# Kernel tuning notes

Hardware: AMD Instinct MI355X
Metric: run time of the kernel (lower is better)

Reference implementation:

```python
import jax, jax.numpy as jnp
import numpy as np

B, S, IN_F, OUT_F = 4, 2048, 4096, 4096
ALPHA = 0.01

def setup_inputs() -> dict:
    key = jax.random.key(0)
    k1, k2 = jax.random.split(key, 2)
    # int8-valued activations and weights (stored as int32 per harness dtype)
    x = jax.random.randint(k1, (B, S, IN_F), -127, 127, dtype=jnp.int32)
    weight = jax.random.randint(k2, (IN_F, OUT_F), -127, 127, dtype=jnp.int32)
    bias = jnp.zeros((1, OUT_F), dtype=jnp.float16)
    alpha = jnp.full((1,), ALPHA, dtype=jnp.float32)
    return {"x": x, "weight": weight, "bias": bias, "alpha": alpha}

def reference(x, weight, bias, alpha):
    # Faithful to forward's default (non-hybrid) path:
    # y = F.linear(x.float(), weight.t().float(), bias.float()) * alpha
    # F.linear(x, W^T) == x @ W, with W shape (in_features, out_features).
    x_shape = x.shape
    xf = x.reshape(-1, x_shape[-1]).astype(jnp.float32)          # [B*S, in]
    wf = weight.astype(jnp.float32)                               # [in, out]
    y = (xf @ wf + bias.astype(jnp.float32)) * alpha              # [B*S, out]
    return y.reshape(*x_shape[:-1], -1)                           # [B, S, out]
```

## Files before the change

kernel.cpp:

```cpp
#include <hip/hip_runtime.h>
#include <hip/hip_fp16.h>

using i32x4  = __attribute__((ext_vector_type(4)))  int;
using i32x16 = __attribute__((ext_vector_type(16))) int;

static constexpr int M  = 4 * 2048;
static constexpr int N  = 4096;
static constexpr int K  = 4096;
static constexpr int BM = 256, BN = 128, BK = 64;
static constexpr int NT = K / BK;
static constexpr int ATILE = BM * BK;
static constexpr int BTILE = BN * BK;


__device__ __forceinline__ unsigned pack4(i32x4 v) {
  return (unsigned)((v.x & 255) | ((v.y & 255) << 8) | ((v.z & 255) << 16) | (v.w << 24));
}

__global__ __launch_bounds__(256) void pack_x_kernel(const int* __restrict__ x,
                                                     unsigned char* __restrict__ wa) {
  unsigned g = blockIdx.x * 256 + threadIdx.x;
  unsigned row = g & 255;
  unsigned kg  = (g >> 8) & 3;
  unsigned kt  = (g >> 10) & 63;
  unsigned br  = g >> 16;
  const int* src = x + ((size_t)(br * 256 + row) * K + kt * 64 + kg * 16);
  i32x4 v0 = *(const i32x4*)(src + 0);
  i32x4 v1 = *(const i32x4*)(src + 4);
  i32x4 v2 = *(const i32x4*)(src + 8);
  i32x4 v3 = *(const i32x4*)(src + 12);
  i32x4 d;
  d.x = (int)pack4(v0); d.y = (int)pack4(v1); d.z = (int)pack4(v2); d.w = (int)pack4(v3);
  *(i32x4*)(wa + (size_t)g * 16) = d;
}

__global__ __launch_bounds__(256) void pack_w_kernel(const int* __restrict__ w,
                                                     unsigned char* __restrict__ wb) {
  unsigned g = blockIdx.x * 256 + threadIdx.x;
  unsigned col = g & 127;
  unsigned kg  = (g >> 7) & 3;
  unsigned kt  = (g >> 9) & 63;
  unsigned bn  = g >> 15;
  unsigned n   = bn * 128 + col;
  unsigned k0  = kt * 64 + kg * 16;
  const int* src = w + (size_t)k0 * N + n;
  i32x4 d;
#pragma unroll
  for (int j = 0; j < 4; ++j) {
    int b0 = src[(size_t)(j * 4 + 0) * N];
    int b1 = src[(size_t)(j * 4 + 1) * N];
    int b2 = src[(size_t)(j * 4 + 2) * N];
    int b3 = src[(size_t)(j * 4 + 3) * N];
    d[j] = (b0 & 255) | ((b1 & 255) << 8) | ((b2 & 255) << 16) | (b3 << 24);
  }
  *(i32x4*)(wb + (size_t)g * 16) = d;
}


__device__ __forceinline__ void gload_lds16(const void* g, void* l) {
  __builtin_amdgcn_global_load_lds((const __attribute__((address_space(1))) unsigned int*)g,
                                   (__attribute__((address_space(3))) unsigned int*)l,
                                   16, 0, 0);
}

__global__ __launch_bounds__(256, 2) void gemm_i8(const unsigned char* __restrict__ wa,
                                                  const unsigned char* __restrict__ wb,
                                                  const __half* __restrict__ bias,
                                                  const float* __restrict__ alphaP,
                                                  float* __restrict__ out) {
  __shared__ __align__(16) unsigned char As[3][ATILE];
  __shared__ __align__(16) unsigned char Bs[3][BTILE];

  const int tid  = threadIdx.x;
  const int lane = tid & 63;
  const int w    = tid >> 6;
  const int wr   = w >> 1, wc = w & 1;
  const int l31  = lane & 31;
  const int kgl  = lane >> 5;

  const int bc = blockIdx.x;
  const int br = blockIdx.y;

  const unsigned char* ga = wa + (size_t)br * NT * ATILE;
  const unsigned char* gb = wb + (size_t)bc * NT * BTILE;

  auto stage = [&](int buf, int t) {
    const unsigned char* at = ga + (size_t)t * ATILE;
    const unsigned char* bt = gb + (size_t)t * BTILE;
#pragma unroll
    for (int j = 0; j < 4; ++j)
      gload_lds16(at + (w * 4 + j) * 1024 + lane * 16, &As[buf][(w * 4 + j) * 1024]);
#pragma unroll
    for (int j = 0; j < 2; ++j)
      gload_lds16(bt + (w * 2 + j) * 1024 + lane * 16, &Bs[buf][(w * 2 + j) * 1024]);
  };

  stage(0, 0);
  stage(1, 1);
  asm volatile("s_waitcnt vmcnt(6)" ::: "memory");
  __builtin_amdgcn_s_barrier();

  i32x16 acc[4][2] = {};

  const int arow = wr * 128 + l31;
  const int bcol = wc * 64 + l31;

  for (int t = 0; t < NT; ++t) {
    if (t + 2 < NT) stage((t + 2) % 3, t + 2);

    const unsigned char* Ab = &As[t % 3][0] + kgl * 4096;
    const unsigned char* Bb = &Bs[t % 3][0] + kgl * 2048;

#pragma unroll
    for (int kc = 0; kc < 2; ++kc) {
      const unsigned char* Ap = Ab + kc * 8192;
      const unsigned char* Bp = Bb + kc * 4096;
      i32x4 a0 = *(const i32x4*)(Ap + (arow +  0) * 16);
      i32x4 a1 = *(const i32x4*)(Ap + (arow + 32) * 16);
      i32x4 a2 = *(const i32x4*)(Ap + (arow + 64) * 16);
      i32x4 a3 = *(const i32x4*)(Ap + (arow + 96) * 16);
      i32x4 b0 = *(const i32x4*)(Bp + (bcol +  0) * 16);
      i32x4 b1 = *(const i32x4*)(Bp + (bcol + 32) * 16);
      acc[0][0] = __builtin_amdgcn_mfma_i32_32x32x32_i8(a0, b0, acc[0][0], 0, 0, 0);
      acc[0][1] = __builtin_amdgcn_mfma_i32_32x32x32_i8(a0, b1, acc[0][1], 0, 0, 0);
      acc[1][0] = __builtin_amdgcn_mfma_i32_32x32x32_i8(a1, b0, acc[1][0], 0, 0, 0);
      acc[1][1] = __builtin_amdgcn_mfma_i32_32x32x32_i8(a1, b1, acc[1][1], 0, 0, 0);
      acc[2][0] = __builtin_amdgcn_mfma_i32_32x32x32_i8(a2, b0, acc[2][0], 0, 0, 0);
      acc[2][1] = __builtin_amdgcn_mfma_i32_32x32x32_i8(a2, b1, acc[2][1], 0, 0, 0);
      acc[3][0] = __builtin_amdgcn_mfma_i32_32x32x32_i8(a3, b0, acc[3][0], 0, 0, 0);
      acc[3][1] = __builtin_amdgcn_mfma_i32_32x32x32_i8(a3, b1, acc[3][1], 0, 0, 0);
    }

    if (t + 2 < NT)      asm volatile("s_waitcnt vmcnt(6)" ::: "memory");
    else if (t + 1 < NT) asm volatile("s_waitcnt vmcnt(0)" ::: "memory");
    __builtin_amdgcn_s_barrier();
  }

  const float alpha = *alphaP;
  const int row0 = br * 256 + wr * 128 + 4 * kgl;
  const int col0 = bc * 128 + wc * 64 + l31;
#pragma unroll
  for (int ni = 0; ni < 2; ++ni) {
    const int col = col0 + ni * 32;
    const float bf = __half2float(bias[col]);
#pragma unroll
    for (int mi = 0; mi < 4; ++mi) {
#pragma unroll
      for (int r = 0; r < 16; ++r) {
        const int row = row0 + mi * 32 + (r & 3) + 8 * (r >> 2);
        out[(size_t)row * N + col] = ((float)acc[mi][ni][r] + bf) * alpha;
      }
    }
  }
}

extern "C" void kernel_launch(void* const* d_in, const int* in_sizes, int n_in,
                              void* d_out, int out_size, void* d_ws, size_t ws_size,
                              hipStream_t stream) {
  const int*    x     = (const int*)d_in[0];
  const int*    wgt   = (const int*)d_in[1];
  const __half* bias  = (const __half*)d_in[2];
  const float*  alpha = (const float*)d_in[3];
  float*        out   = (float*)d_out;

  unsigned char* wa = (unsigned char*)d_ws;
  unsigned char* wb = wa + (size_t)M * K;

  pack_x_kernel<<<(M * (size_t)K / 16) / 256, 256, 0, stream>>>(x, wa);
  pack_w_kernel<<<(N * (size_t)K / 16) / 256, 256, 0, stream>>>(wgt, wb);

  dim3 grid(N / BN, M / BM);
  gemm_i8<<<grid, 256, 0, stream>>>(wa, wb, bias, alpha, out);
}
```

Measured before the change: 242.4 us.

## Replace direct-to-LDS triple buffering with register-staged double buffering; merge pack kernels

```diff
diff --git a/kernel.cpp b/kernel.cpp
--- a/kernel.cpp
+++ b/kernel.cpp
@@ -12,64 +12,61 @@
 static constexpr int ATILE = BM * BK;
 static constexpr int BTILE = BN * BK;
 
+static constexpr int PX_BLOCKS = (int)((size_t)M * K / 16 / 256);
+static constexpr int PW_BLOCKS = (int)((size_t)N * K / 16 / 256);
 
 __device__ __forceinline__ unsigned pack4(i32x4 v) {
   return (unsigned)((v.x & 255) | ((v.y & 255) << 8) | ((v.z & 255) << 16) | (v.w << 24));
 }
 
-__global__ __launch_bounds__(256) void pack_x_kernel(const int* __restrict__ x,
-                                                     unsigned char* __restrict__ wa) {
-  unsigned g = blockIdx.x * 256 + threadIdx.x;
-  unsigned row = g & 255;
-  unsigned kg  = (g >> 8) & 3;
-  unsigned kt  = (g >> 10) & 63;
-  unsigned br  = g >> 16;
-  const int* src = x + ((size_t)(br * 256 + row) * K + kt * 64 + kg * 16);
-  i32x4 v0 = *(const i32x4*)(src + 0);
-  i32x4 v1 = *(const i32x4*)(src + 4);
-  i32x4 v2 = *(const i32x4*)(src + 8);
-  i32x4 v3 = *(const i32x4*)(src + 12);
-  i32x4 d;
-  d.x = (int)pack4(v0); d.y = (int)pack4(v1); d.z = (int)pack4(v2); d.w = (int)pack4(v3);
-  *(i32x4*)(wa + (size_t)g * 16) = d;
+__global__ __launch_bounds__(256) void pack_kernel(const int* __restrict__ x,
+                                                   const int* __restrict__ w,
+                                                   unsigned char* __restrict__ wa,
+                                                   unsigned char* __restrict__ wb) {
+  if (blockIdx.x < PX_BLOCKS) {
+    unsigned g = blockIdx.x * 256 + threadIdx.x;
+    unsigned row = g & 255;
+    unsigned kg  = (g >> 8) & 3;
+    unsigned kt  = (g >> 10) & 63;
+    unsigned br  = g >> 16;
+    const int* src = x + ((size_t)(br * 256 + row) * K + kt * 64 + kg * 16);
+    i32x4 v0 = *(const i32x4*)(src + 0);
+    i32x4 v1 = *(const i32x4*)(src + 4);
+    i32x4 v2 = *(const i32x4*)(src + 8);
+    i32x4 v3 = *(const i32x4*)(src + 12);
+    i32x4 d;
+    d.x = (int)pack4(v0); d.y = (int)pack4(v1); d.z = (int)pack4(v2); d.w = (int)pack4(v3);
+    *(i32x4*)(wa + (size_t)g * 16) = d;
+  } else {
+    unsigned g = (blockIdx.x - PX_BLOCKS) * 256 + threadIdx.x;
+    unsigned col = g & 127;
+    unsigned kg  = (g >> 7) & 3;
+    unsigned kt  = (g >> 9) & 63;
+    unsigned bn  = g >> 15;
+    unsigned n   = bn * 128 + col;
+    unsigned k0  = kt * 64 + kg * 16;
+    const int* src = w + (size_t)k0 * N + n;
+    i32x4 d;
+#pragma unroll
+    for (int j = 0; j < 4; ++j) {
+      int b0 = src[(size_t)(j * 4 + 0) * N];
+      int b1 = src[(size_t)(j * 4 + 1) * N];
+      int b2 = src[(size_t)(j * 4 + 2) * N];
+      int b3 = src[(size_t)(j * 4 + 3) * N];
+      d[j] = (b0 & 255) | ((b1 & 255) << 8) | ((b2 & 255) << 16) | (b3 << 24);
+    }
+    *(i32x4*)(wb + (size_t)g * 16) = d;
+  }
 }
 
-__global__ __launch_bounds__(256) void pack_w_kernel(const int* __restrict__ w,
-                                                     unsigned char* __restrict__ wb) {
-  unsigned g = blockIdx.x * 256 + threadIdx.x;
-  unsigned col = g & 127;
-  unsigned kg  = (g >> 7) & 3;
-  unsigned kt  = (g >> 9) & 63;
-  unsigned bn  = g >> 15;
-  unsigned n   = bn * 128 + col;
-  unsigned k0  = kt * 64 + kg * 16;
-  const int* src = w + (size_t)k0 * N + n;
-  i32x4 d;
-#pragma unroll
-  for (int j = 0; j < 4; ++j) {
-    int b0 = src[(size_t)(j * 4 + 0) * N];
-    int b1 = src[(size_t)(j * 4 + 1) * N];
-    int b2 = src[(size_t)(j * 4 + 2) * N];
-    int b3 = src[(size_t)(j * 4 + 3) * N];
-    d[j] = (b0 & 255) | ((b1 & 255) << 8) | ((b2 & 255) << 16) | (b3 << 24);
-  }
-  *(i32x4*)(wb + (size_t)g * 16) = d;
-}
-
-
-__device__ __forceinline__ void gload_lds16(const void* g, void* l) {
-  __builtin_amdgcn_global_load_lds((const __attribute__((address_space(1))) unsigned int*)g,
-                                   (__attribute__((address_space(3))) unsigned int*)l,
-                                   16, 0, 0);
-}
 
 __global__ __launch_bounds__(256, 2) void gemm_i8(const unsigned char* __restrict__ wa,
                                                   const unsigned char* __restrict__ wb,
                                                   const __half* __restrict__ bias,
                                                   const float* __restrict__ alphaP,
                                                   float* __restrict__ out) {
-  __shared__ __align__(16) unsigned char As[3][ATILE];
-  __shared__ __align__(16) unsigned char Bs[3][BTILE];
+  __shared__ __align__(16) unsigned char As[2][ATILE];
+  __shared__ __align__(16) unsigned char Bs[2][BTILE];
 
   const int tid  = threadIdx.x;
   const int lane = tid & 63;
@@ -84,21 +81,27 @@
   const unsigned char* ga = wa + (size_t)br * NT * ATILE;
   const unsigned char* gb = wb + (size_t)bc * NT * BTILE;
 
-  auto stage = [&](int buf, int t) {
-    const unsigned char* at = ga + (size_t)t * ATILE;
-    const unsigned char* bt = gb + (size_t)t * BTILE;
-#pragma unroll
-    for (int j = 0; j < 4; ++j)
-      gload_lds16(at + (w * 4 + j) * 1024 + lane * 16, &As[buf][(w * 4 + j) * 1024]);
-#pragma unroll
-    for (int j = 0; j < 2; ++j)
-      gload_lds16(bt + (w * 2 + j) * 1024 + lane * 16, &Bs[buf][(w * 2 + j) * 1024]);
-  };
+  i32x4 s0, s1, s2, s3, s4, s5;
 
-  stage(0, 0);
-  stage(1, 1);
-  asm volatile("s_waitcnt vmcnt(6)" ::: "memory");
-  __builtin_amdgcn_s_barrier();
+#define GLOAD(T) do {                                                \
+    const i32x4* ap = (const i32x4*)(ga + (size_t)(T) * ATILE);      \
+    const i32x4* bp = (const i32x4*)(gb + (size_t)(T) * BTILE);      \
+    s0 = ap[tid]; s1 = ap[tid + 256];                                \
+    s2 = ap[tid + 512]; s3 = ap[tid + 768];                          \
+    s4 = bp[tid]; s5 = bp[tid + 256];                                \
+  } while (0)
+
+#define SWRITE(BUF) do {                                             \
+    i32x4* aw = (i32x4*)&As[BUF][0];                                 \
+    i32x4* bw = (i32x4*)&Bs[BUF][0];                                 \
+    aw[tid] = s0; aw[tid + 256] = s1;                                \
+    aw[tid + 512] = s2; aw[tid + 768] = s3;                          \
+    bw[tid] = s4; bw[tid + 256] = s5;                                \
+  } while (0)
+
+  GLOAD(0);
+  SWRITE(0);
+  __syncthreads();
 
   i32x16 acc[4][2] = {};
 
@@ -106,11 +109,11 @@
   const int bcol = wc * 64 + l31;
 
   for (int t = 0; t < NT; ++t) {
-    if (t + 2 < NT) stage((t + 2) % 3, t + 2);
+    const int cur = t & 1;
+    if (t + 1 < NT) GLOAD(t + 1);
 
-    const unsigned char* Ab = &As[t % 3][0] + kgl * 4096;
-    const unsigned char* Bb = &Bs[t % 3][0] + kgl * 2048;
-
+    const unsigned char* Ab = &As[cur][0] + kgl * 4096;
+    const unsigned char* Bb = &Bs[cur][0] + kgl * 2048;
 #pragma unroll
     for (int kc = 0; kc < 2; ++kc) {
       const unsigned char* Ap = Ab + kc * 8192;
@@ -131,9 +134,9 @@
       acc[3][1] = __builtin_amdgcn_mfma_i32_32x32x32_i8(a3, b1, acc[3][1], 0, 0, 0);
     }
 
-    if (t + 2 < NT)      asm volatile("s_waitcnt vmcnt(6)" ::: "memory");
-    else if (t + 1 < NT) asm volatile("s_waitcnt vmcnt(0)" ::: "memory");
-    __builtin_amdgcn_s_barrier();
+    __builtin_amdgcn_sched_barrier(0);
+    if (t + 1 < NT) SWRITE(cur ^ 1);
+    __syncthreads();
   }
 
   const float alpha = *alphaP;
@@ -152,6 +155,8 @@
       }
     }
   }
+#undef GLOAD
+#undef SWRITE
 }
 
 extern "C" void kernel_launch(void* const* d_in, const int* in_sizes, int n_in,
@@ -166,8 +171,7 @@
   unsigned char* wa = (unsigned char*)d_ws;
   unsigned char* wb = wa + (size_t)M * K;
 
-  pack_x_kernel<<<(M * (size_t)K / 16) / 256, 256, 0, stream>>>(x, wa);
-  pack_w_kernel<<<(N * (size_t)K / 16) / 256, 256, 0, stream>>>(wgt, wb);
+  pack_kernel<<<PX_BLOCKS + PW_BLOCKS, 256, 0, stream>>>(x, wgt, wa, wb);
 
   dim3 grid(N / BN, M / BM);
   gemm_i8<<<grid, 256, 0, stream>>>(wa, wb, bias, alpha, out);
```

Measured after the change: 229.2 us. 1.06x faster.
